# Optimization experiments

Measured on AMD Instinct MI355X. Metric: run time of the kernel, lower is better.

Reference implementation:

```python
import jax, jax.numpy as jnp
import numpy as np

NB, DIM, DSTATE, DCONV, EXPAND = 4, 256, 16, 4, 2
DIN = EXPAND * DIM                 # 512
DTRANK = (DIM + 15) // 16          # 16, mamba-ssm default dt_rank = ceil(d_model/16)
B, L = 16, 512


def layer_norm(x, w, b, eps=1e-5):
    mu = x.mean(-1, keepdims=True)
    var = x.var(-1, keepdims=True)
    return (x - mu) * jax.lax.rsqrt(var + eps) * w + b


def selective_scan(u, delta, A, Bm, Cm, D):
    # u, delta: (B,L,DIN); Bm,Cm: (B,L,N); A: (DIN,N); D: (DIN,)
    def step(h, xs):
        d_t, B_t, C_t, u_t = xs          # (B,DIN), (B,N), (B,N), (B,DIN)
        dA = jnp.exp(d_t[..., None] * A)                                  # (B,DIN,N)
        h = dA * h + d_t[..., None] * B_t[:, None, :] * u_t[..., None]   # (B,DIN,N)
        y = jnp.einsum('bdn,bn->bd', h, C_t)
        return h, y

    h0 = jnp.zeros((u.shape[0], u.shape[2], A.shape[1]), u.dtype)
    xs = (delta.transpose(1, 0, 2), Bm.transpose(1, 0, 2),
          Cm.transpose(1, 0, 2), u.transpose(1, 0, 2))
    _, ys = jax.lax.scan(step, h0, xs)
    return ys.transpose(1, 0, 2) + u * D


def mamba_block(x, ln_w, ln_b, in_w, in_b, cw, cb, xp_w, dtw, dtb, A_log, D, ow):
    h = layer_norm(x, ln_w, ln_b)
    xz = h @ in_w.T + in_b                       # (B,L,2*DIN)
    xin, z = xz[..., :DIN], xz[..., DIN:]
    # causal depthwise conv over the sequence dim
    xc = jax.lax.conv_general_dilated(
        xin.transpose(0, 2, 1), cw[:, None, :], (1,), [(DCONV - 1, 0)],
        dimension_numbers=('NCH', 'OIH', 'NCH'), feature_group_count=DIN)
    xc = jax.nn.silu(xc + cb[None, :, None]).transpose(0, 2, 1)   # (B,L,DIN)
    dbc = xc @ xp_w.T                                             # (B,L,DTRANK+2*N)
    dt = jax.nn.softplus(dbc[..., :DTRANK] @ dtw.T + dtb)         # (B,L,DIN)
    Bm = dbc[..., DTRANK:DTRANK + DSTATE]
    Cm = dbc[..., DTRANK + DSTATE:]
    y = selective_scan(xc, dt, -jnp.exp(A_log), Bm, Cm, D)
    return x + (y * jax.nn.silu(z)) @ ow.T       # dropout = identity at eval


def setup_inputs() -> dict:
    key = jax.random.key(0)
    ks = jax.random.split(key, 8)
    s = 0.02
    A_log = jnp.tile(jnp.log(jnp.arange(1, DSTATE + 1, dtype=jnp.float32))[None, None, :],
                     (NB, DIN, 1))
    return {
        'x': jax.random.normal(ks[0], (B, L, DIM), jnp.float32),
        'ln_w': jnp.ones((NB, DIM), jnp.float32),
        'ln_b': jnp.zeros((NB, DIM), jnp.float32),
        'in_proj_w': jax.random.normal(ks[1], (NB, 2 * DIN, DIM), jnp.float32) * s,
        'in_proj_b': jnp.zeros((NB, 2 * DIN), jnp.float32),
        'conv_w': jax.random.normal(ks[2], (NB, DIN, DCONV), jnp.float32) * s,
        'conv_b': jnp.zeros((NB, DIN), jnp.float32),
        'x_proj_w': jax.random.normal(ks[3], (NB, DTRANK + 2 * DSTATE, DIN), jnp.float32) * s,
        'dt_proj_w': jax.random.normal(ks[4], (NB, DIN, DTRANK), jnp.float32) * s,
        'dt_proj_b': jax.random.uniform(ks[5], (NB, DIN), jnp.float32, -4.0, -3.0),
        'A_log': A_log,
        'D': jnp.ones((NB, DIN), jnp.float32),
        'out_proj_w': jax.random.normal(ks[6], (NB, DIM, DIN), jnp.float32) * s,
    }


def reference(x, ln_w, ln_b, in_proj_w, in_proj_b, conv_w, conv_b, x_proj_w,
              dt_proj_w, dt_proj_b, A_log, D, out_proj_w):
    for i in range(NB):
        x = mamba_block(x, ln_w[i], ln_b[i], in_proj_w[i], in_proj_b[i],
                        conv_w[i], conv_b[i], x_proj_w[i], dt_proj_w[i],
                        dt_proj_b[i], A_log[i], D[i], out_proj_w[i])
    return x
```

## Files before the change

### kernel.cpp

```cpp
#include <hip/hip_runtime.h>
#include <math.h>

#define NB 4
#define DIMM 256
#define DSTATE 16
#define DCONV 4
#define DIN 512
#define DTRANK 16
#define BB 16
#define LL 512
#define TT (BB * LL)
#define XZ_DIM (2 * DIN)
#define DBC_DIM (DTRANK + 2 * DSTATE)
#define NC 16
#define CHUNK (LL / NC)

__device__ __forceinline__ unsigned short f2bf(float f) {
    union { float f; unsigned int u; } v; v.f = f;
    unsigned int r = v.u + 0x7fff + ((v.u >> 16) & 1);
    return (unsigned short)(r >> 16);
}
__device__ __forceinline__ float bf2f(unsigned short u) {
    union { unsigned int i; float f; } v; v.i = ((unsigned int)u) << 16;
    return v.f;
}

__global__ __launch_bounds__(256) void cvt3_kernel(const float* __restrict__ s1,
                                                   unsigned short* __restrict__ d1, int n1,
                                                   const float* __restrict__ s2,
                                                   unsigned short* __restrict__ d2, int n2,
                                                   const float* __restrict__ s3,
                                                   unsigned short* __restrict__ d3, int n3) {
    int stride = gridDim.x * 256;
    for (int i = blockIdx.x * 256 + threadIdx.x; i < n1; i += stride) {
        float4 v = ((const float4*)s1)[i];
        ushort4 o; o.x = f2bf(v.x); o.y = f2bf(v.y); o.z = f2bf(v.z); o.w = f2bf(v.w);
        ((ushort4*)d1)[i] = o;
    }
    for (int i = blockIdx.x * 256 + threadIdx.x; i < n2; i += stride) {
        float4 v = ((const float4*)s2)[i];
        ushort4 o; o.x = f2bf(v.x); o.y = f2bf(v.y); o.z = f2bf(v.z); o.w = f2bf(v.w);
        ((ushort4*)d2)[i] = o;
    }
    for (int i = blockIdx.x * 256 + threadIdx.x; i < n3; i += stride) {
        float4 v = ((const float4*)s3)[i];
        ushort4 o; o.x = f2bf(v.x); o.y = f2bf(v.y); o.z = f2bf(v.z); o.w = f2bf(v.w);
        ((ushort4*)d3)[i] = o;
    }
}

__global__ __launch_bounds__(256) void ln_kernel(const float* __restrict__ x,
                                                 const float* __restrict__ w,
                                                 const float* __restrict__ bvec,
                                                 unsigned short* __restrict__ out) {
    int t = blockIdx.x;
    int i = threadIdx.x;
    float v = x[t * DIMM + i];
    float s = v, s2 = v * v;
#pragma unroll
    for (int off = 1; off < 64; off <<= 1) {
        s  += __shfl_xor(s, off);
        s2 += __shfl_xor(s2, off);
    }
    __shared__ float ss[4], ss2[4];
    int wid = i >> 6;
    if ((i & 63) == 0) { ss[wid] = s; ss2[wid] = s2; }
    __syncthreads();
    s  = ss[0] + ss[1] + ss[2] + ss[3];
    s2 = ss2[0] + ss2[1] + ss2[2] + ss2[3];
    float mu  = s * (1.0f / DIMM);
    float var = s2 * (1.0f / DIMM) - mu * mu;
    float r   = rsqrtf(var + 1e-5f);
    out[t * DIMM + i] = f2bf((v - mu) * r * w[i] + bvec[i]);
}

#define TBM 128
#define TBN 64
#define TBK 32
#define LDKW (TBK + 8)
__global__ __launch_bounds__(256) void gemm_bf16(const unsigned short* __restrict__ A, int lda,
                                                 const unsigned short* __restrict__ Bw, int ldb,
                                                 const float* __restrict__ bias,
                                                 const float* __restrict__ resid,
                                                 float* __restrict__ C,
                                                 unsigned short* __restrict__ C1b,
                                                 unsigned short* __restrict__ C2b, int nsplit,
                                                 int ldc, int N, int K) {
    using short8  = __attribute__((ext_vector_type(8))) short;
    using floatx4 = __attribute__((ext_vector_type(4))) float;
    __shared__ __align__(16) unsigned short As[TBM * LDKW];
    __shared__ __align__(16) unsigned short Bs[TBN * LDKW];

    int tid  = threadIdx.x;
    int m0   = blockIdx.y * TBM;
    int n0   = blockIdx.x * TBN;
    int w    = tid >> 6;
    int lane = tid & 63;
    int wm   = (w & 1) * 64;
    int wn   = (w >> 1) * 32;
    int lr   = lane & 15;
    int quad = lane >> 4;

    floatx4 acc[4][2] = {};

    int ar = tid >> 1;
    int ak = (tid & 1) * 16;
    int br = tid >> 2;
    int bk = (tid & 3) * 8;

    for (int k0 = 0; k0 < K; k0 += TBK) {
        {
            const unsigned short* src = &A[(size_t)(m0 + ar) * lda + k0 + ak];
            int4 a0 = *(const int4*)(src);
            int4 a1 = *(const int4*)(src + 8);
            *(int4*)&As[ar * LDKW + ak]     = a0;
            *(int4*)&As[ar * LDKW + ak + 8] = a1;
        }
        {
            int gn = n0 + br;
            int4 b0 = make_int4(0, 0, 0, 0);
            if (gn < N) b0 = *(const int4*)&Bw[(size_t)gn * ldb + k0 + bk];
            *(int4*)&Bs[br * LDKW + bk] = b0;
        }
        __syncthreads();
        short8 af[4], bf[2];
#pragma unroll
        for (int i = 0; i < 4; ++i)
            af[i] = *(const short8*)&As[(wm + i * 16 + lr) * LDKW + quad * 8];
#pragma unroll
        for (int j = 0; j < 2; ++j)
            bf[j] = *(const short8*)&Bs[(wn + j * 16 + lr) * LDKW + quad * 8];
#pragma unroll
        for (int i = 0; i < 4; ++i)
#pragma unroll
            for (int j = 0; j < 2; ++j)
                acc[i][j] = __builtin_amdgcn_mfma_f32_16x16x32_bf16(af[i], bf[j], acc[i][j], 0, 0, 0);
        __syncthreads();
    }

#pragma unroll
    for (int j = 0; j < 2; ++j) {
        int cn = n0 + wn + j * 16 + lr;
        if (cn < N) {
            float bb = bias ? bias[cn] : 0.0f;
            if (C1b) {
                unsigned short* dst = (cn < nsplit) ? C1b : C2b;
                int col = (cn < nsplit) ? cn : cn - nsplit;
#pragma unroll
                for (int i = 0; i < 4; ++i)
#pragma unroll
                    for (int r = 0; r < 4; ++r) {
                        int cm = m0 + wm + i * 16 + quad * 4 + r;
                        dst[(size_t)cm * ldc + col] = f2bf(acc[i][j][r] + bb);
                    }
            } else {
#pragma unroll
                for (int i = 0; i < 4; ++i)
#pragma unroll
                    for (int r = 0; r < 4; ++r) {
                        int cm = m0 + wm + i * 16 + quad * 4 + r;
                        float v = acc[i][j][r] + bb;
                        if (resid) v += resid[(size_t)cm * ldc + cn];
                        C[(size_t)cm * ldc + cn] = v;
                    }
            }
        }
    }
}

__global__ __launch_bounds__(256) void conv_silu(const unsigned short* __restrict__ Xb,
                                                 const float* __restrict__ cw,
                                                 const float* __restrict__ cb,
                                                 unsigned short* __restrict__ xcb) {
    int idx = blockIdx.x * blockDim.x + threadIdx.x;
    int d = idx & (DIN - 1);
    int t = idx >> 9;
    int l = t & (LL - 1);
    int bq = t >> 9;
    float acc = cb[d];
#pragma unroll
    for (int k = 0; k < DCONV; ++k) {
        int ls = l - (DCONV - 1) + k;
        if (ls >= 0) acc += cw[d * DCONV + k] * bf2f(Xb[(size_t)(bq * LL + ls) * DIN + d]);
    }
    float v = acc / (1.0f + __expf(-acc));
    xcb[(size_t)t * DIN + d] = f2bf(v);
}

__global__ __launch_bounds__(256) void scan_p1(const unsigned short* __restrict__ xcb,
                                               const float* __restrict__ dbc,
                                               const float* __restrict__ A_log,
                                               const float* __restrict__ dtw,
                                               const float* __restrict__ dtbias,
                                               unsigned short* __restrict__ dtb,
                                               float* __restrict__ S,
                                               float* __restrict__ H) {
    int bid = blockIdx.x;
    int dq = bid & 3;
    int c  = (bid >> 2) & (NC - 1);
    int b  = bid >> 6;
    int dloc = threadIdx.x >> 1;
    int sh   = threadIdx.x & 1;
    int d  = dq * 128 + dloc;
    int n0 = sh * 8;
    int base = b * LL + c * CHUNK;

    __shared__ float LB[CHUNK * DBC_DIM];
    for (int i = threadIdx.x; i < CHUNK * DBC_DIM / 4; i += 256)
        ((float4*)LB)[i] = ((const float4*)(dbc + (size_t)base * DBC_DIM))[i];

    float a[8], wv16[16];
    {
        const float4* ar = (const float4*)(A_log + d * DSTATE + n0);
        float4 v0 = ar[0], v1 = ar[1];
        a[0] = -__expf(v0.x); a[1] = -__expf(v0.y); a[2] = -__expf(v0.z); a[3] = -__expf(v0.w);
        a[4] = -__expf(v1.x); a[5] = -__expf(v1.y); a[6] = -__expf(v1.z); a[7] = -__expf(v1.w);
        const float4* wr = (const float4*)(dtw + d * DTRANK);
#pragma unroll
        for (int q = 0; q < 4; ++q) {
            float4 ww = wr[q];
            wv16[q * 4 + 0] = ww.x; wv16[q * 4 + 1] = ww.y;
            wv16[q * 4 + 2] = ww.z; wv16[q * 4 + 3] = ww.w;
        }
    }
    float db = dtbias[d];
    __syncthreads();

    float h[8];
#pragma unroll
    for (int j = 0; j < 8; ++j) h[j] = 0.0f;
    float Ssum = 0.0f;
    float u = bf2f(xcb[(size_t)base * DIN + d]);
#pragma unroll 4
    for (int s = 0; s < CHUNK; ++s) {
        float nu = bf2f(xcb[(size_t)(base + s + 1) * DIN + d]);
        const float* row = &LB[s * DBC_DIM];
        float dot = db;
#pragma unroll
        for (int k = 0; k < 16; ++k) dot += row[k] * wv16[k];
        float dtv = (dot > 20.0f) ? dot : log1pf(__expf(dot));
        if (sh == 0) dtb[(size_t)(base + s) * DIN + d] = f2bf(dtv);
        Ssum += dtv;
        float wv = dtv * u;
#pragma unroll
        for (int j = 0; j < 8; ++j) {
            float dA = __expf(dtv * a[j]);
            h[j] = dA * h[j] + wv * row[DTRANK + n0 + j];
        }
        u = nu;
    }
    size_t sc = (size_t)b * NC + c;
    if (sh == 0) S[sc * DIN + d] = Ssum;
#pragma unroll
    for (int j = 0; j < 8; ++j) H[(sc * DIN + d) * 16 + n0 + j] = h[j];
}

__global__ __launch_bounds__(256) void scan_p2(const float* __restrict__ A_log,
                                               const float* __restrict__ S,
                                               float* __restrict__ H) {
    int idx = blockIdx.x * 256 + threadIdx.x;
    int n = idx & 15;
    int d = (idx >> 4) & (DIN - 1);
    int b = idx >> 13;
    float a = -__expf(A_log[d * DSTATE + n]);
    float h = 0.0f;
#pragma unroll
    for (int c = 0; c < NC; ++c) {
        size_t sc = (size_t)b * NC + c;
        float Sv = S[sc * DIN + d];
        size_t q = (sc * DIN + d) * 16 + n;
        float Hc = H[q];
        H[q] = h;
        h = __expf(a * Sv) * h + Hc;
    }
}

__global__ __launch_bounds__(256) void scan_p3(const unsigned short* __restrict__ xcb,
                                               const unsigned short* __restrict__ dtb,
                                               const unsigned short* __restrict__ Zb,
                                               const float* __restrict__ dbc,
                                               const float* __restrict__ A_log,
                                               const float* __restrict__ Dp,
                                               const float* __restrict__ Hin,
                                               unsigned short* __restrict__ gb) {
    int bid = blockIdx.x;
    int dq = bid & 3;
    int c  = (bid >> 2) & (NC - 1);
    int b  = bid >> 6;
    int dloc = threadIdx.x >> 1;
    int sh   = threadIdx.x & 1;
    int d  = dq * 128 + dloc;
    int n0 = sh * 8;
    int base = b * LL + c * CHUNK;

    __shared__ float LB[CHUNK * DBC_DIM];
    for (int i = threadIdx.x; i < CHUNK * DBC_DIM / 4; i += 256)
        ((float4*)LB)[i] = ((const float4*)(dbc + (size_t)base * DBC_DIM))[i];

    float a[8];
    {
        const float4* ar = (const float4*)(A_log + d * DSTATE + n0);
        float4 v0 = ar[0], v1 = ar[1];
        a[0] = -__expf(v0.x); a[1] = -__expf(v0.y); a[2] = -__expf(v0.z); a[3] = -__expf(v0.w);
        a[4] = -__expf(v1.x); a[5] = -__expf(v1.y); a[6] = -__expf(v1.z); a[7] = -__expf(v1.w);
    }
    float Dd = Dp[d];
    size_t sc = (size_t)b * NC + c;
    float h[8];
#pragma unroll
    for (int j = 0; j < 8; ++j) h[j] = Hin[(sc * DIN + d) * 16 + n0 + j];
    __syncthreads();

    float u   = bf2f(xcb[(size_t)base * DIN + d]);
    float dtv = bf2f(dtb[(size_t)base * DIN + d]);
#pragma unroll 4
    for (int s = 0; s < CHUNK; ++s) {
        float nu  = bf2f(xcb[(size_t)(base + s + 1) * DIN + d]);
        float ndt = bf2f(dtb[(size_t)(base + s + 1) * DIN + d]);
        const float* row = &LB[s * DBC_DIM];
        float wv = dtv * u;
        float y  = (sh == 0) ? u * Dd : 0.0f;
#pragma unroll
        for (int j = 0; j < 8; ++j) {
            float dA = __expf(dtv * a[j]);
            h[j] = dA * h[j] + wv * row[DTRANK + n0 + j];
            y += h[j] * row[DTRANK + DSTATE + n0 + j];
        }
        y += __shfl_xor(y, 1);
        if (sh == 0) {
            float zf = bf2f(Zb[(size_t)(base + s) * DIN + d]);
            float g = y * (zf / (1.0f + __expf(-zf)));
            gb[(size_t)(base + s) * DIN + d] = f2bf(g);
        }
        u = nu; dtv = ndt;
    }
}

extern "C" void kernel_launch(void* const* d_in, const int* in_sizes, int n_in,
                              void* d_out, int out_size, void* d_ws, size_t ws_size,
                              hipStream_t stream) {
    const float* x_in   = (const float*)d_in[0];
    const float* ln_w   = (const float*)d_in[1];
    const float* ln_b   = (const float*)d_in[2];
    const float* in_w   = (const float*)d_in[3];
    const float* in_b   = (const float*)d_in[4];
    const float* conv_w = (const float*)d_in[5];
    const float* conv_b = (const float*)d_in[6];
    const float* xp_w   = (const float*)d_in[7];
    const float* dt_w   = (const float*)d_in[8];
    const float* dt_b   = (const float*)d_in[9];
    const float* A_log  = (const float*)d_in[10];
    const float* Dp     = (const float*)d_in[11];
    const float* ow     = (const float*)d_in[12];
    float* out = (float*)d_out;

    const size_t M = 1048576;
    float* ws = (float*)d_ws;
    float* xbuf = ws;
    unsigned short* hb  = (unsigned short*)(ws + 2 * M);
    float* dbc = ws + 3 * M;
    unsigned short* Xb  = (unsigned short*)(ws + 4 * M);
    unsigned short* Zb  = (unsigned short*)(ws + 6 * M);
    unsigned short* xcb = (unsigned short*)(ws + 8 * M);
    unsigned short* dtb = (unsigned short*)(ws + 10 * M);
    unsigned short* gb  = (unsigned short*)(ws + 12 * M);
    float* Hbuf = ws + 14 * M;
    float* Sbuf = ws + 16 * M;
    unsigned short* inwb = (unsigned short*)(ws + 17 * M);
    unsigned short* owb  = inwb + (size_t)NB * XZ_DIM * DIMM;
    unsigned short* xpwb = owb + (size_t)NB * DIMM * DIN;

    cvt3_kernel<<<256, 256, 0, stream>>>(
        in_w, inwb, NB * XZ_DIM * DIMM / 4,
        ow,   owb,  NB * DIMM * DIN / 4,
        xp_w, xpwb, NB * DBC_DIM * DIN / 4);

    for (int layer = 0; layer < NB; ++layer) {
        const float* xi = (layer == 0) ? x_in : xbuf;
        float* xo = (layer == NB - 1) ? out : xbuf;

        ln_kernel<<<TT, 256, 0, stream>>>(xi, ln_w + layer * DIMM, ln_b + layer * DIMM, hb);

        gemm_bf16<<<dim3(XZ_DIM / TBN, TT / TBM), 256, 0, stream>>>(
            hb, DIMM, inwb + (size_t)layer * XZ_DIM * DIMM, DIMM,
            in_b + layer * XZ_DIM, nullptr, nullptr, Xb, Zb, DIN, DIN, XZ_DIM, DIMM);

        conv_silu<<<(TT * DIN) / 256, 256, 0, stream>>>(
            Xb, conv_w + layer * DIN * DCONV, conv_b + layer * DIN, xcb);

        gemm_bf16<<<dim3(1, TT / TBM), 256, 0, stream>>>(
            xcb, DIN, xpwb + (size_t)layer * DBC_DIM * DIN, DIN,
            nullptr, nullptr, dbc, nullptr, nullptr, 0, DBC_DIM, DBC_DIM, DIN);

        const float* Al  = A_log + (size_t)layer * DIN * DSTATE;
        const float* dwl = dt_w + (size_t)layer * DIN * DTRANK;
        const float* dbl = dt_b + layer * DIN;
        scan_p1<<<BB * NC * 4, 256, 0, stream>>>(xcb, dbc, Al, dwl, dbl, dtb, Sbuf, Hbuf);
        scan_p2<<<(BB * DIN * 16) / 256, 256, 0, stream>>>(Al, Sbuf, Hbuf);
        scan_p3<<<BB * NC * 4, 256, 0, stream>>>(xcb, dtb, Zb, dbc, Al,
                                                 Dp + layer * DIN, Hbuf, gb);

        gemm_bf16<<<dim3(DIMM / TBN, TT / TBM), 256, 0, stream>>>(
            gb, DIN, owb + (size_t)layer * DIMM * DIN, DIN,
            nullptr, xi, xo, nullptr, nullptr, 0, DIMM, DIMM, DIN);
    }
}
```

Before: 714.4 us.

## Split dt projection into its own kernel and double scan chunk count

Moves the dt projection plus softplus out of scan_p1 into a separate fully parallel dt_kernel that writes bf16 dt. scan_p1 now reads the precomputed dt instead of recomputing it and storing it. The number of scan chunks is doubled, which halves the sequential chunk length and doubles block count for scan_p1/p3, and the workspace layout is enlarged for the bigger H buffer. The cost is an extra kernel launch and extra memory traffic for dt, plus a longer inter-chunk pass in scan_p2. scan_p1 also now uses the bf16-rounded dt, so its state accumulation differs slightly in precision from before.

```diff
diff --git a/kernel.cpp b/kernel.cpp
--- a/kernel.cpp
+++ b/kernel.cpp
@@ -12,7 +12,7 @@
 #define TT (BB * LL)
 #define XZ_DIM (2 * DIN)
 #define DBC_DIM (DTRANK + 2 * DSTATE)
-#define NC 16
+#define NC 32
 #define CHUNK (LL / NC)
 
 __device__ __forceinline__ unsigned short f2bf(float f) {
@@ -187,18 +187,36 @@
     xcb[(size_t)t * DIN + d] = f2bf(v);
 }
 
+__global__ __launch_bounds__(256) void dt_kernel(const float* __restrict__ dbc,
+                                                 const float* __restrict__ dtw,
+                                                 const float* __restrict__ dtbias,
+                                                 unsigned short* __restrict__ dtout) {
+    int idx = blockIdx.x * blockDim.x + threadIdx.x;
+    int d = idx & (DIN - 1);
+    int t = idx >> 9;
+    float a = dtbias[d];
+    const float4* wv = (const float4*)(dtw + d * DTRANK);
+    const float* dr = dbc + (size_t)t * DBC_DIM;
+#pragma unroll
+    for (int q = 0; q < 4; ++q) {
+        float4 w4 = wv[q];
+        a += w4.x * dr[q * 4 + 0] + w4.y * dr[q * 4 + 1] +
+             w4.z * dr[q * 4 + 2] + w4.w * dr[q * 4 + 3];
+    }
+    float sp = (a > 20.0f) ? a : log1pf(__expf(a));
+    dtout[(size_t)t * DIN + d] = f2bf(sp);
+}
+
 __global__ __launch_bounds__(256) void scan_p1(const unsigned short* __restrict__ xcb,
+                                               const unsigned short* __restrict__ dtb,
                                                const float* __restrict__ dbc,
                                                const float* __restrict__ A_log,
-                                               const float* __restrict__ dtw,
-                                               const float* __restrict__ dtbias,
-                                               unsigned short* __restrict__ dtb,
                                                float* __restrict__ S,
                                                float* __restrict__ H) {
     int bid = blockIdx.x;
     int dq = bid & 3;
     int c  = (bid >> 2) & (NC - 1);
-    int b  = bid >> 6;
+    int b  = bid >> 7;
     int dloc = threadIdx.x >> 1;
     int sh   = threadIdx.x & 1;
     int d  = dq * 128 + dloc;
@@ -209,37 +227,26 @@
     for (int i = threadIdx.x; i < CHUNK * DBC_DIM / 4; i += 256)
         ((float4*)LB)[i] = ((const float4*)(dbc + (size_t)base * DBC_DIM))[i];
 
-    float a[8], wv16[16];
+    float a[8];
     {
         const float4* ar = (const float4*)(A_log + d * DSTATE + n0);
         float4 v0 = ar[0], v1 = ar[1];
         a[0] = -__expf(v0.x); a[1] = -__expf(v0.y); a[2] = -__expf(v0.z); a[3] = -__expf(v0.w);
         a[4] = -__expf(v1.x); a[5] = -__expf(v1.y); a[6] = -__expf(v1.z); a[7] = -__expf(v1.w);
-        const float4* wr = (const float4*)(dtw + d * DTRANK);
-#pragma unroll
-        for (int q = 0; q < 4; ++q) {
-            float4 ww = wr[q];
-            wv16[q * 4 + 0] = ww.x; wv16[q * 4 + 1] = ww.y;
-            wv16[q * 4 + 2] = ww.z; wv16[q * 4 + 3] = ww.w;
-        }
-    }
-    float db = dtbias[d];
+    }
     __syncthreads();
 
     float h[8];
 #pragma unroll
     for (int j = 0; j < 8; ++j) h[j] = 0.0f;
     float Ssum = 0.0f;
-    float u = bf2f(xcb[(size_t)base * DIN + d]);
+    float u   = bf2f(xcb[(size_t)base * DIN + d]);
+    float dtv = bf2f(dtb[(size_t)base * DIN + d]);
 #pragma unroll 4
     for (int s = 0; s < CHUNK; ++s) {
-        float nu = bf2f(xcb[(size_t)(base + s + 1) * DIN + d]);
+        float nu  = bf2f(xcb[(size_t)(base + s + 1) * DIN + d]);
+        float ndt = bf2f(dtb[(size_t)(base + s + 1) * DIN + d]);
         const float* row = &LB[s * DBC_DIM];
-        float dot = db;
-#pragma unroll
-        for (int k = 0; k < 16; ++k) dot += row[k] * wv16[k];
-        float dtv = (dot > 20.0f) ? dot : log1pf(__expf(dot));
-        if (sh == 0) dtb[(size_t)(base + s) * DIN + d] = f2bf(dtv);
         Ssum += dtv;
         float wv = dtv * u;
 #pragma unroll
@@ -247,7 +254,7 @@
             float dA = __expf(dtv * a[j]);
             h[j] = dA * h[j] + wv * row[DTRANK + n0 + j];
         }
-        u = nu;
+        u = nu; dtv = ndt;
     }
     size_t sc = (size_t)b * NC + c;
     if (sh == 0) S[sc * DIN + d] = Ssum;
@@ -286,7 +293,7 @@
     int bid = blockIdx.x;
     int dq = bid & 3;
     int c  = (bid >> 2) & (NC - 1);
-    int b  = bid >> 6;
+    int b  = bid >> 7;
     int dloc = threadIdx.x >> 1;
     int sh   = threadIdx.x & 1;
     int d  = dq * 128 + dloc;
@@ -365,8 +372,8 @@
     unsigned short* dtb = (unsigned short*)(ws + 10 * M);
     unsigned short* gb  = (unsigned short*)(ws + 12 * M);
     float* Hbuf = ws + 14 * M;
-    float* Sbuf = ws + 16 * M;
-    unsigned short* inwb = (unsigned short*)(ws + 17 * M);
+    float* Sbuf = ws + 18 * M;
+    unsigned short* inwb = (unsigned short*)(ws + 18 * M + 262144);
     unsigned short* owb  = inwb + (size_t)NB * XZ_DIM * DIMM;
     unsigned short* xpwb = owb + (size_t)NB * DIMM * DIN;
 
@@ -392,10 +399,11 @@
             xcb, DIN, xpwb + (size_t)layer * DBC_DIM * DIN, DIN,
             nullptr, nullptr, dbc, nullptr, nullptr, 0, DBC_DIM, DBC_DIM, DIN);
 
-        const float* Al  = A_log + (size_t)layer * DIN * DSTATE;
-        const float* dwl = dt_w + (size_t)layer * DIN * DTRANK;
-        const float* dbl = dt_b + layer * DIN;
-        scan_p1<<<BB * NC * 4, 256, 0, stream>>>(xcb, dbc, Al, dwl, dbl, dtb, Sbuf, Hbuf);
+        dt_kernel<<<(TT * DIN) / 256, 256, 0, stream>>>(
+            dbc, dt_w + (size_t)layer * DIN * DTRANK, dt_b + layer * DIN, dtb);
+
+        const float* Al = A_log + (size_t)layer * DIN * DSTATE;
+        scan_p1<<<BB * NC * 4, 256, 0, stream>>>(xcb, dtb, dbc, Al, Sbuf, Hbuf);
         scan_p2<<<(BB * DIN * 16) / 256, 256, 0, stream>>>(Al, Sbuf, Hbuf);
         scan_p3<<<BB * NC * 4, 256, 0, stream>>>(xcb, dtb, Zb, dbc, Al,
                                                  Dp + layer * DIN, Hbuf, gb);
```

Measured after the change: 688.9 us. 1.04x faster.
